# Performance work log

Measured on AMD Instinct MI355X. Metric: run time of the kernel, lower is better.

Reference implementation:

```python
import jax, jax.numpy as jnp
import numpy as np

H, D, E, S_E, P_E, N, B = 16, 48, 768, 384, 128, 768, 1

def _ln(x, g=None, b=None, eps=1e-5):
    mu = jnp.mean(x, axis=-1, keepdims=True)
    var = jnp.var(x, axis=-1, keepdims=True)
    y = (x - mu) * jax.lax.rsqrt(var + eps)
    if g is not None:
        y = y * g
    if b is not None:
        y = y + b
    return y

def setup_inputs() -> dict:
    key = jax.random.key(0)
    ks = jax.random.split(key, 16)
    sc_e = 1.0 / np.sqrt(E)
    sc_s = 1.0 / np.sqrt(S_E)
    sc_p = 1.0 / np.sqrt(P_E)
    return {
        "a": jax.random.normal(ks[0], (B, N, E), jnp.float32),
        "s": jax.random.normal(ks[1], (B, N, S_E), jnp.float32),
        "pair_rep": jax.random.normal(ks[2], (B, N, N, P_E), jnp.float32),
        "beta": jax.random.normal(ks[3], (B, N, N), jnp.float32),
        # AdaLN: sigmoid-gated scale and shift from s
        "w_ada_gamma": jax.random.normal(ks[4], (S_E, E), jnp.float32) * sc_s,
        "w_ada_beta": jax.random.normal(ks[5], (S_E, E), jnp.float32) * sc_s,
        # q/k/v projections, stored as [E, H, D]
        "wq": jax.random.normal(ks[6], (E, H, D), jnp.float32) * sc_e,
        "bq": jnp.zeros((H, D), jnp.float32),
        "wk": jax.random.normal(ks[7], (E, H, D), jnp.float32) * sc_e,
        "wv": jax.random.normal(ks[8], (E, H, D), jnp.float32) * sc_e,
        # pair bias: LayerNorm(P_E) + Linear(P_E -> H, no bias)
        "ln_pair_g": jnp.ones((P_E,), jnp.float32),
        "ln_pair_b": jnp.zeros((P_E,), jnp.float32),
        "w_pair": jax.random.normal(ks[9], (P_E, H), jnp.float32) * sc_p,
        # gate projection [E, H, D], no bias, sigmoid
        "w_gate": jax.random.normal(ks[10], (E, H, D), jnp.float32) * sc_e,
        # output projections
        "w_proj_a": jax.random.normal(ks[11], (E, E), jnp.float32) * sc_e,
        "w_out": jax.random.normal(ks[12], (S_E, E), jnp.float32) * sc_s,
        "b_out": jnp.full((E,), -2.0, jnp.float32),
    }

def reference(a, s, pair_rep, beta, w_ada_gamma, w_ada_beta, wq, bq, wk, wv,
              ln_pair_g, ln_pair_b, w_pair, w_gate, w_proj_a, w_out, b_out):
    # AdaLN: normalize a (no affine); gamma/beta conditioned on normalized s
    a_n = _ln(a)
    s_n = _ln(s)
    gamma = jax.nn.sigmoid(s_n @ w_ada_gamma)
    a_mod = gamma * a_n + s_n @ w_ada_beta            # [B,N,E]

    q = jnp.einsum('bne,ehd->bnhd', a_mod, wq) + bq   # [B,N,H,D]
    k = jnp.einsum('bne,ehd->bnhd', a_mod, wk)
    v = jnp.einsum('bne,ehd->bnhd', a_mod, wv)
    g = jax.nn.sigmoid(jnp.einsum('bne,ehd->bnhd', a_mod, w_gate))

    # per-head pair bias: LN(pair) @ w_pair + beta -> [B,H,N,N]
    b = jnp.einsum('bnmp,ph->bhnm', _ln(pair_rep, ln_pair_g, ln_pair_b), w_pair)
    b = b + beta[:, None, :, :]

    scale = 1.0 / np.sqrt(D)
    logits = jnp.einsum('bnhd,bmhd->bhnm', q, k) * scale + b
    weights = jax.nn.softmax(logits, axis=-1)         # [B,H,N,N]

    attn = jnp.einsum('bhnm,bmhd->bhnd', weights, v)
    attn = attn * jnp.moveaxis(g, -2, -3)             # gate per head
    attn = jnp.moveaxis(attn, -3, -2).reshape(a.shape[0], a.shape[1], H * D)
    out = attn @ w_proj_a                             # [B,N,E]
    out = jax.nn.sigmoid(s @ w_out + b_out) * out
    return out
```

## Files before the change

### kernel.cpp

```cpp
#include <hip/hip_runtime.h>
#include <hip/hip_bf16.h>

typedef __attribute__((ext_vector_type(8))) short short8;
typedef __attribute__((ext_vector_type(8))) unsigned short u16x8;
typedef __attribute__((ext_vector_type(4))) unsigned short u16x4;
typedef __attribute__((ext_vector_type(4))) float f32x4;
typedef __attribute__((ext_vector_type(4))) unsigned u32x4;

#define NTOK 768
#define ED   768
#define SD   384
#define PD   128
#define NH   16
#define DH   48
#define LGS  778

__device__ __forceinline__ unsigned short f2bf(float x) {
  unsigned u = __builtin_bit_cast(unsigned, x);
  u += 0x7FFFu + ((u >> 16) & 1u);
  return (unsigned short)(u >> 16);
}
__device__ __forceinline__ float bf2f(unsigned short b) {
  unsigned u = ((unsigned)b) << 16;
  return __builtin_bit_cast(float, u);
}
__device__ __forceinline__ float sigm(float x) { return 1.0f / (1.0f + __expf(-x)); }

__device__ __forceinline__ unsigned cvtpk(float a, float b) {
  unsigned r;
  asm("v_cvt_pk_bf16_f32 %0, %1, %2" : "=v"(r) : "v"(a), "v"(b));
  return r;
}
__device__ __forceinline__ float lo2f(unsigned p) {
  return __builtin_bit_cast(float, p << 16);
}
__device__ __forceinline__ float hi2f(unsigned p) {
  return __builtin_bit_cast(float, p & 0xFFFF0000u);
}

__device__ __forceinline__ void gl2lds(const unsigned short* g, unsigned short* l) {
  __builtin_amdgcn_global_load_lds(
      (const __attribute__((address_space(1))) unsigned int*)g,
      (__attribute__((address_space(3))) unsigned int*)l, 16, 0, 0);
}

constexpr size_t SZ_SN   = (size_t)NTOK * SD * 2;
constexpr size_t OFF_SNH = 0;
constexpr size_t OFF_SNL = OFF_SNH + SZ_SN;
constexpr size_t OFF_SRH = OFF_SNL + SZ_SN;
constexpr size_t OFF_SRL = OFF_SRH + SZ_SN;
constexpr size_t OFF_GAM = OFF_SRL + SZ_SN;
constexpr size_t OFF_BET = OFF_GAM + 2359296;
constexpr size_t OFF_OG  = OFF_BET + 2359296;
constexpr size_t OFF_AMH = OFF_OG  + 2359296;
constexpr size_t OFF_AML = OFF_AMH + 1179648;
constexpr size_t OFF_QB  = OFF_AML + 1179648;
constexpr size_t OFF_KB  = OFF_QB  + 1179648;
constexpr size_t OFF_VT  = OFF_KB  + 1179648;
constexpr size_t OFF_GBUF= OFF_VT  + 1179648;
constexpr size_t OFF_AGH = OFF_GBUF+ 2359296;
constexpr size_t OFF_AGL = OFF_AGH + 1179648;
constexpr size_t OFF_WSMH= OFF_AGL + 1179648;
constexpr size_t OFF_WSML= OFF_WSMH+ 1769472;
constexpr size_t OFF_WQH = OFF_WSML+ 1769472;
constexpr size_t OFF_WQL = OFF_WQH + 4718592;
constexpr size_t OFF_WPH = OFF_WQL + 4718592;
constexpr size_t OFF_WPL = OFF_WPH + 1179648;
constexpr size_t OFF_GWH = OFF_WPL + 1179648;
constexpr size_t OFF_GWL = OFF_GWH + 4096;
constexpr size_t OFF_SGW = OFF_GWL + 4096;
constexpr size_t OFF_QKL = OFF_SGW + 4096;
constexpr size_t OFF_PB  = OFF_QKL + 37748736;
constexpr size_t WS_NEED = OFF_PB  + 18874368;

__global__ __launch_bounds__(256) void k_wcvt(
    const float* __restrict__ wag, const float* __restrict__ wab, const float* __restrict__ wo,
    const float* __restrict__ wq, const float* __restrict__ wk, const float* __restrict__ wv,
    const float* __restrict__ wg, const float* __restrict__ wp,
    const float* __restrict__ lng, const float* __restrict__ lnb,
    const float* __restrict__ wpair, const float* __restrict__ s,
    unsigned short* __restrict__ wsmh, unsigned short* __restrict__ wsml,
    unsigned short* __restrict__ wqh, unsigned short* __restrict__ wql,
    unsigned short* __restrict__ wph, unsigned short* __restrict__ wpl,
    unsigned short* __restrict__ gwh, unsigned short* __restrict__ gwl,
    float* __restrict__ sgw, float* __restrict__ bw,
    unsigned short* __restrict__ snh, unsigned short* __restrict__ snl,
    unsigned short* __restrict__ srh, unsigned short* __restrict__ srl) {
  const int tid = threadIdx.x;
  if (blockIdx.z == 8) {
    const int gid = blockIdx.y * 24 + blockIdx.x;
    if (gid == 192) {
      if (tid < 128) {
        float g = lng[tid];
        for (int hh = 0; hh < 16; ++hh) {
          float gwv = g * wpair[tid * 16 + hh];
          unsigned short hb = f2bf(gwv);
          gwh[tid * 16 + hh] = hb;
          gwl[tid * 16 + hh] = f2bf(gwv - bf2f(hb));
        }
      }
      if (tid < 16) {
        float sv = 0.f, bb = 0.f;
        for (int p = 0; p < 128; ++p) {
          float w = wpair[p * 16 + tid];
          sv += lng[p] * w;
          bb += lnb[p] * w;
        }
        sgw[tid] = sv;
        bw[tid]  = bb;
      }
      return;
    }
    if (gid > 192) return;
    const int n = gid * 4 + (tid >> 6);
    const int lane = tid & 63;
    const float* row = s + (size_t)n * SD;
    float v[6], sum = 0.f, sq = 0.f;
#pragma unroll
    for (int i = 0; i < 6; ++i) { v[i] = row[lane + 64 * i]; sum += v[i]; sq += v[i] * v[i]; }
#pragma unroll
    for (int off = 1; off < 64; off <<= 1) { sum += __shfl_xor(sum, off); sq += __shfl_xor(sq, off); }
    float mu = sum * (1.f / SD);
    float var = sq * (1.f / SD) - mu * mu;
    float rs = rsqrtf(var + 1e-5f);
#pragma unroll
    for (int i = 0; i < 6; ++i) {
      size_t idx = (size_t)n * SD + lane + 64 * i;
      float x = v[i];
      unsigned short xh = f2bf(x);
      srh[idx] = xh; srl[idx] = f2bf(x - bf2f(xh));
      float y = (x - mu) * rs;
      unsigned short yh = f2bf(y);
      snh[idx] = yh; snl[idx] = f2bf(y - bf2f(yh));
    }
    return;
  }
  const int id = blockIdx.z;
  const float* src; int Ksrc; unsigned short *dh, *dl; int n0; int Kd;
  switch (id) {
    case 0: src = wag; Ksrc = 384; dh = wsmh; dl = wsml; n0 = 0;    Kd = 384; break;
    case 1: src = wab; Ksrc = 384; dh = wsmh; dl = wsml; n0 = 768;  Kd = 384; break;
    case 2: src = wo;  Ksrc = 384; dh = wsmh; dl = wsml; n0 = 1536; Kd = 384; break;
    case 3: src = wq;  Ksrc = 768; dh = wqh;  dl = wql;  n0 = 0;    Kd = 768; break;
    case 4: src = wk;  Ksrc = 768; dh = wqh;  dl = wql;  n0 = 768;  Kd = 768; break;
    case 5: src = wv;  Ksrc = 768; dh = wqh;  dl = wql;  n0 = 1536; Kd = 768; break;
    case 6: src = wg;  Ksrc = 768; dh = wqh;  dl = wql;  n0 = 2304; Kd = 768; break;
    default: src = wp; Ksrc = 768; dh = wph;  dl = wpl;  n0 = 0;    Kd = 768; break;
  }
  const int kt = blockIdx.x, ntile = blockIdx.y;
  if (kt * 32 >= Ksrc) return;
  __shared__ float t[32][33];
  const int r = tid >> 3, c4 = (tid & 7) * 4;
  float4 v = *(const float4*)(src + (size_t)(kt * 32 + r) * 768 + ntile * 32 + c4);
  t[r][c4 + 0] = v.x; t[r][c4 + 1] = v.y; t[r][c4 + 2] = v.z; t[r][c4 + 3] = v.w;
  __syncthreads();
  u16x4 hv, lv;
#pragma unroll
  for (int j = 0; j < 4; ++j) {
    float x = t[c4 + j][r];
    unsigned short hb = f2bf(x);
    hv[j] = hb;
    lv[j] = f2bf(x - bf2f(hb));
  }
  size_t drow = (size_t)(n0 + ntile * 32 + r) * Kd + kt * 32 + c4;
  *(u16x4*)(dh + drow) = hv;
  *(u16x4*)(dl + drow) = lv;
}

__device__ __forceinline__ void mfma_core(
    const unsigned short* __restrict__ Ah, const unsigned short* __restrict__ Al,
    const unsigned short* __restrict__ Bh, const unsigned short* __restrict__ Bl,
    int K, int mBase, int nBase, f32x4 acc[2][2]) {
  __shared__ unsigned short lds[2][4][4096];
  const int tid = threadIdx.x;
  const int w = tid >> 6, lane = tid & 63;
  const int l15 = lane & 15, kg = lane >> 4;
  const int wr = w >> 1, wc = w & 1;

  size_t offA[2], offB[2];
  int ldsw[2];
#pragma unroll
  for (int i = 0; i < 2; ++i) {
    int chunk = w * 128 + i * 64 + lane;
    int row = chunk >> 3;
    int slot = (chunk & 7) ^ (row & 7);
    offA[i] = (size_t)(mBase + row) * K + slot * 8;
    offB[i] = (size_t)(nBase + row) * K + slot * 8;
    ldsw[i] = w * 1024 + i * 512;
  }
  auto stage = [&](int b, int k0) {
#pragma unroll
    for (int i = 0; i < 2; ++i) {
      gl2lds(Ah + offA[i] + k0, &lds[b][0][ldsw[i]]);
      gl2lds(Al + offA[i] + k0, &lds[b][1][ldsw[i]]);
      gl2lds(Bh + offB[i] + k0, &lds[b][2][ldsw[i]]);
      gl2lds(Bl + offB[i] + k0, &lds[b][3][ldsw[i]]);
    }
  };

  stage(0, 0);
  int buf = 0;
  for (int k0 = 64; k0 <= K; k0 += 64) {
    __syncthreads();
    if (k0 < K) stage(buf ^ 1, k0);
#pragma unroll
    for (int kk = 0; kk < 2; ++kk) {
      short8 ah[2], al[2], bh4[2], bl4[2];
#pragma unroll
      for (int mi = 0; mi < 2; ++mi) {
        int row = wr * 32 + mi * 16 + l15;
        int kb = kk * 64 + kg * 16;
        int idx = row * 64 + ((kb ^ ((row & 7) << 4)) >> 1);
        ah[mi] = *(const short8*)&lds[buf][0][idx];
        al[mi] = *(const short8*)&lds[buf][1][idx];
      }
#pragma unroll
      for (int ni = 0; ni < 2; ++ni) {
        int row = wc * 32 + ni * 16 + l15;
        int kb = kk * 64 + kg * 16;
        int idx = row * 64 + ((kb ^ ((row & 7) << 4)) >> 1);
        bh4[ni] = *(const short8*)&lds[buf][2][idx];
        bl4[ni] = *(const short8*)&lds[buf][3][idx];
      }
#pragma unroll
      for (int mi = 0; mi < 2; ++mi)
#pragma unroll
        for (int ni = 0; ni < 2; ++ni) {
          acc[mi][ni] = __builtin_amdgcn_mfma_f32_16x16x32_bf16(ah[mi], bh4[ni], acc[mi][ni], 0, 0, 0);
          acc[mi][ni] = __builtin_amdgcn_mfma_f32_16x16x32_bf16(al[mi], bh4[ni], acc[mi][ni], 0, 0, 0);
          acc[mi][ni] = __builtin_amdgcn_mfma_f32_16x16x32_bf16(ah[mi], bl4[ni], acc[mi][ni], 0, 0, 0);
        }
    }
    buf ^= 1;
  }
}

__global__ __launch_bounds__(256) void k_gemm_small(
    const unsigned short* __restrict__ snh, const unsigned short* __restrict__ snl,
    const unsigned short* __restrict__ srh, const unsigned short* __restrict__ srl,
    const unsigned short* __restrict__ wsmh, const unsigned short* __restrict__ wsml,
    const float* __restrict__ bo,
    float* __restrict__ gaml, float* __restrict__ betl, float* __restrict__ og) {
  const int nt = blockIdx.x, mt = blockIdx.y;
  const unsigned short* Ah = (nt < 24) ? snh : srh;
  const unsigned short* Al = (nt < 24) ? snl : srl;
  f32x4 acc[2][2];
#pragma unroll
  for (int i = 0; i < 2; ++i)
#pragma unroll
    for (int j = 0; j < 2; ++j) acc[i][j] = (f32x4){0.f, 0.f, 0.f, 0.f};
  mfma_core(Ah, Al, wsmh, wsml, SD, mt * 64, nt * 64, acc);
  const int tid = threadIdx.x;
  const int w = tid >> 6, lane = tid & 63;
  const int l15 = lane & 15, kg = lane >> 4;
  const int wr = w >> 1, wc = w & 1;
#pragma unroll
  for (int mi = 0; mi < 2; ++mi)
#pragma unroll
    for (int ni = 0; ni < 2; ++ni) {
      int col = nt * 64 + wc * 32 + ni * 16 + l15;
#pragma unroll
      for (int r = 0; r < 4; ++r) {
        int row = mt * 64 + wr * 32 + mi * 16 + kg * 4 + r;
        float v = acc[mi][ni][r];
        if (col < 768) gaml[(size_t)row * ED + col] = v;
        else if (col < 1536) betl[(size_t)row * ED + col - 768] = v;
        else og[(size_t)row * ED + col - 1536] = sigm(v + bo[col - 1536]);
      }
    }
}

__global__ __launch_bounds__(256) void k_gemm_qkvg(
    const unsigned short* __restrict__ amh, const unsigned short* __restrict__ aml,
    const unsigned short* __restrict__ wqh, const unsigned short* __restrict__ wql,
    const float* __restrict__ bq,
    unsigned short* __restrict__ qb, unsigned short* __restrict__ kb,
    unsigned short* __restrict__ vT, float* __restrict__ gbuf) {
  const int nt = blockIdx.x, mt = blockIdx.y;
  f32x4 acc[2][2];
#pragma unroll
  for (int i = 0; i < 2; ++i)
#pragma unroll
    for (int j = 0; j < 2; ++j) acc[i][j] = (f32x4){0.f, 0.f, 0.f, 0.f};
  mfma_core(amh, aml, wqh, wql, ED, mt * 64, nt * 64, acc);
  const int tid = threadIdx.x;
  const int w = tid >> 6, lane = tid & 63;
  const int l15 = lane & 15, kg = lane >> 4;
  const int wr = w >> 1, wc = w & 1;
  const int sel = nt / 12;
#pragma unroll
  for (int mi = 0; mi < 2; ++mi)
#pragma unroll
    for (int ni = 0; ni < 2; ++ni) {
      int col = nt * 64 + wc * 32 + ni * 16 + l15;
      int c = col - sel * 768;
#pragma unroll
      for (int r = 0; r < 4; ++r) {
        int row = mt * 64 + wr * 32 + mi * 16 + kg * 4 + r;
        float v = acc[mi][ni][r];
        size_t idx = (size_t)row * ED + c;
        if (sel == 0) qb[idx] = f2bf(v + bq[c]);
        else if (sel == 1) kb[idx] = f2bf(v);
        else if (sel == 2) vT[(size_t)c * NTOK + row] = f2bf(v);
        else gbuf[idx] = sigm(v);
      }
    }
}

__global__ __launch_bounds__(256) void k_gemm_proj(
    const unsigned short* __restrict__ agh, const unsigned short* __restrict__ agl,
    const unsigned short* __restrict__ wph, const unsigned short* __restrict__ wpl,
    const float* __restrict__ og, float* __restrict__ out) {
  const int nt = blockIdx.x, mt = blockIdx.y;
  f32x4 acc[2][2];
#pragma unroll
  for (int i = 0; i < 2; ++i)
#pragma unroll
    for (int j = 0; j < 2; ++j) acc[i][j] = (f32x4){0.f, 0.f, 0.f, 0.f};
  mfma_core(agh, agl, wph, wpl, ED, mt * 64, nt * 64, acc);
  const int tid = threadIdx.x;
  const int w = tid >> 6, lane = tid & 63;
  const int l15 = lane & 15, kg = lane >> 4;
  const int wr = w >> 1, wc = w & 1;
#pragma unroll
  for (int mi = 0; mi < 2; ++mi)
#pragma unroll
    for (int ni = 0; ni < 2; ++ni) {
      int col = nt * 64 + wc * 32 + ni * 16 + l15;
#pragma unroll
      for (int r = 0; r < 4; ++r) {
        int row = mt * 64 + wr * 32 + mi * 16 + kg * 4 + r;
        size_t idx = (size_t)row * ED + col;
        out[idx] = acc[mi][ni][r] * og[idx];
      }
    }
}

__global__ __launch_bounds__(256) void k_amod(const float* __restrict__ a,
                                              const float* __restrict__ gamma_lin,
                                              const float* __restrict__ beta_lin,
                                              unsigned short* __restrict__ amh,
                                              unsigned short* __restrict__ aml) {
  __shared__ float red[8];
  const int n = blockIdx.x, tid = threadIdx.x;
  const int lane = tid & 63, wid = tid >> 6;
  const float* row = a + (size_t)n * ED;
  float v[3], sum = 0.f, sq = 0.f;
#pragma unroll
  for (int i = 0; i < 3; ++i) { v[i] = row[tid + 256 * i]; sum += v[i]; sq += v[i] * v[i]; }
#pragma unroll
  for (int off = 1; off < 64; off <<= 1) { sum += __shfl_xor(sum, off); sq += __shfl_xor(sq, off); }
  if (lane == 0) { red[wid] = sum; red[4 + wid] = sq; }
  __syncthreads();
  float S = red[0] + red[1] + red[2] + red[3];
  float Q = red[4] + red[5] + red[6] + red[7];
  float mu = S * (1.f / ED);
  float var = Q * (1.f / ED) - mu * mu;
  float rs = rsqrtf(var + 1e-5f);
#pragma unroll
  for (int i = 0; i < 3; ++i) {
    int e = tid + 256 * i;
    float an = (v[i] - mu) * rs;
    size_t idx = (size_t)n * ED + e;
    float val = sigm(gamma_lin[idx]) * an + beta_lin[idx];
    unsigned short h = f2bf(val);
    amh[idx] = h;
    aml[idx] = f2bf(val - bf2f(h));
  }
}

__global__ __launch_bounds__(256) void k_qkw(const unsigned short* __restrict__ qb,
                                             const unsigned short* __restrict__ kb,
                                             const float* __restrict__ beta,
                                             float* __restrict__ qkl) {
  const int mt = blockIdx.x, ntile = blockIdx.y, h = blockIdx.z;
  __shared__ unsigned short qs[64 * 72];
  __shared__ unsigned short ksm[64 * 72];
  const int tid = threadIdx.x;
  const int n0 = ntile * 64, m0 = mt * 64;
  const u16x8 z = {0, 0, 0, 0, 0, 0, 0, 0};
#pragma unroll
  for (int it = 0; it < 2; ++it) {
    int idx = tid + it * 256;
    int row = idx >> 3, c = idx & 7;
    u16x8 vq = z, vk = z;
    if (c < 6) {
      vq = *(const u16x8*)(qb + (size_t)(n0 + row) * ED + h * DH + c * 8);
      vk = *(const u16x8*)(kb + (size_t)(m0 + row) * ED + h * DH + c * 8);
    }
    *(u16x8*)(qs + row * 72 + c * 8) = vq;
    *(u16x8*)(ksm + row * 72 + c * 8) = vk;
  }
  __syncthreads();
  const int wv = tid >> 6, lane = tid & 63;
  const int l15 = lane & 15, kg = lane >> 4;
  f32x4 acc[4];
#pragma unroll
  for (int ct = 0; ct < 4; ++ct) acc[ct] = (f32x4){0.f, 0.f, 0.f, 0.f};
#pragma unroll
  for (int ks2 = 0; ks2 < 2; ++ks2) {
    short8 av = *(const short8*)(qs + (wv * 16 + l15) * 72 + ks2 * 32 + kg * 8);
#pragma unroll
    for (int ct = 0; ct < 4; ++ct) {
      short8 bv = *(const short8*)(ksm + (ct * 16 + l15) * 72 + ks2 * 32 + kg * 8);
      acc[ct] = __builtin_amdgcn_mfma_f32_16x16x32_bf16(av, bv, acc[ct], 0, 0, 0);
    }
  }
  const float scale = 0.14433756729740643f;
#pragma unroll
  for (int ct = 0; ct < 4; ++ct)
#pragma unroll
    for (int r = 0; r < 4; ++r) {
      int nn = n0 + wv * 16 + kg * 4 + r;
      int mm = m0 + ct * 16 + l15;
      qkl[((size_t)nn * NH + h) * NTOK + mm] =
          fmaf(acc[ct][r], scale, beta[(size_t)nn * NTOK + mm]);
    }
}

__global__ __launch_bounds__(256, 3) void k_pairsm(const float* __restrict__ pair_rep,
                                                   const float* __restrict__ qkl,
                                                   const unsigned short* __restrict__ gw_hi,
                                                   const unsigned short* __restrict__ gw_lo,
                                                   const float* __restrict__ sgw, const float* __restrict__ bw,
                                                   unsigned short* __restrict__ pb) {
  __shared__ float lg[16 * LGS];
  const int n = blockIdx.x;
  const int tid = threadIdx.x;
  const int wv = tid >> 6, lane = tid & 63;
  const int l15 = lane & 15, kg = lane >> 4;

#define LOADCH(X, CH) do {                                                        \
    const float* xp_ = pair_rep + ((size_t)n * NTOK + (CH) * 16 + l15) * PD + kg * 8; \
    _Pragma("unroll")                                                             \
    for (int q_ = 0; q_ < 4; ++q_) {                                              \
      X[q_ * 2]     = *(const float4*)(xp_ + q_ * 32);                            \
      X[q_ * 2 + 1] = *(const float4*)(xp_ + q_ * 32 + 4);                        \
    }                                                                             \
  } while (0)

  float4 Xa[8], Xb[8];
  LOADCH(Xa, wv);
  LOADCH(Xb, wv + 4);

  short8 bh[4], bl[4];
#pragma unroll
  for (int ks = 0; ks < 4; ++ks)
#pragma unroll
    for (int j = 0; j < 8; ++j) {
      int p = ks * 32 + kg * 8 + j;
      bh[ks][j] = (short)gw_hi[p * 16 + l15];
      bl[ks][j] = (short)gw_lo[p * 16 + l15];
    }
  float sgv[4], bwv[4];
#pragma unroll
  for (int r = 0; r < 4; ++r) { sgv[r] = sgw[kg * 4 + r]; bwv[r] = bw[kg * 4 + r]; }

#define PROC(X, CH) do {                                                          \
    float sum_ = 0.f, sq_ = 0.f;                                                  \
    _Pragma("unroll")                                                             \
    for (int q_ = 0; q_ < 8; ++q_) {                                              \
      sum_ += X[q_].x + X[q_].y + X[q_].z + X[q_].w;                              \
      sq_ = fmaf(X[q_].x, X[q_].x, sq_); sq_ = fmaf(X[q_].y, X[q_].y, sq_);       \
      sq_ = fmaf(X[q_].z, X[q_].z, sq_); sq_ = fmaf(X[q_].w, X[q_].w, sq_);       \
    }                                                                             \
    sum_ += __shfl_xor(sum_, 16); sum_ += __shfl_xor(sum_, 32);                   \
    sq_  += __shfl_xor(sq_, 16);  sq_  += __shfl_xor(sq_, 32);                    \
    float mu_ = sum_ * (1.f / 128.f);                                             \
    float rstd_ = rsqrtf(sq_ * (1.f / 128.f) - mu_ * mu_ + 1e-5f);                \
    f32x4 acc_ = {0.f, 0.f, 0.f, 0.f};                                            \
    _Pragma("unroll")                                                             \
    for (int ks_ = 0; ks_ < 4; ++ks_) {                                           \
      float4 u0_ = X[ks_ * 2], u1_ = X[ks_ * 2 + 1];                              \
      unsigned p0_ = cvtpk(u0_.x, u0_.y), p1_ = cvtpk(u0_.z, u0_.w);              \
      unsigned p2_ = cvtpk(u1_.x, u1_.y), p3_ = cvtpk(u1_.z, u1_.w);              \
      float l0_ = u0_.x - lo2f(p0_), l1_ = u0_.y - hi2f(p0_);                     \
      float l2_ = u0_.z - lo2f(p1_), l3_ = u0_.w - hi2f(p1_);                     \
      float l4_ = u1_.x - lo2f(p2_), l5_ = u1_.y - hi2f(p2_);                     \
      float l6_ = u1_.z - lo2f(p3_), l7_ = u1_.w - hi2f(p3_);                     \
      unsigned q0_ = cvtpk(l0_, l1_), q1_ = cvtpk(l2_, l3_);                      \
      unsigned q2_ = cvtpk(l4_, l5_), q3_ = cvtpk(l6_, l7_);                      \
      u32x4 hp_ = {p0_, p1_, p2_, p3_}, lp_ = {q0_, q1_, q2_, q3_};               \
      short8 ah_ = __builtin_bit_cast(short8, hp_);                               \
      short8 al_ = __builtin_bit_cast(short8, lp_);                               \
      acc_ = __builtin_amdgcn_mfma_f32_16x16x32_bf16(bh[ks_], ah_, acc_, 0, 0, 0);\
      acc_ = __builtin_amdgcn_mfma_f32_16x16x32_bf16(bh[ks_], al_, acc_, 0, 0, 0);\
      acc_ = __builtin_amdgcn_mfma_f32_16x16x32_bf16(bl[ks_], ah_, acc_, 0, 0, 0);\
    }                                                                             \
    _Pragma("unroll")                                                             \
    for (int r_ = 0; r_ < 4; ++r_) {                                              \
      float val_ = rstd_ * (acc_[r_] - mu_ * sgv[r_]) + bwv[r_];                  \
      lg[(kg * 4 + r_) * LGS + (CH) * 16 + l15] = val_;                           \
    }                                                                             \
  } while (0)

  PROC(Xa, wv +  0); LOADCH(Xa, wv +  8);
  PROC(Xb, wv +  4); LOADCH(Xb, wv + 12);
  PROC(Xa, wv +  8); LOADCH(Xa, wv + 16);
  PROC(Xb, wv + 12); LOADCH(Xb, wv + 20);
  PROC(Xa, wv + 16); LOADCH(Xa, wv + 24);
  PROC(Xb, wv + 20); LOADCH(Xb, wv + 28);
  PROC(Xa, wv + 24); LOADCH(Xa, wv + 32);
  PROC(Xb, wv + 28); LOADCH(Xb, wv + 36);
  PROC(Xa, wv + 32); LOADCH(Xa, wv + 40);
  PROC(Xb, wv + 36); LOADCH(Xb, wv + 44);
  PROC(Xa, wv + 40);
  PROC(Xb, wv + 44);
#undef LOADCH
#undef PROC
  __syncthreads();

#pragma unroll
  for (int hh = 0; hh < 4; ++hh) {
    int h = wv * 4 + hh;
    const float* qrow = qkl + ((size_t)n * NH + h) * NTOK;
    float x[12];
#pragma unroll
    for (int i = 0; i < 12; ++i) x[i] = lg[h * LGS + lane + 64 * i] + qrow[lane + 64 * i];
    float mx = x[0];
#pragma unroll
    for (int t = 1; t < 12; ++t) mx = fmaxf(mx, x[t]);
#pragma unroll
    for (int off = 1; off < 64; off <<= 1) mx = fmaxf(mx, __shfl_xor(mx, off));
    float e[12], sm = 0.f;
#pragma unroll
    for (int t = 0; t < 12; ++t) { e[t] = __expf(x[t] - mx); sm += e[t]; }
#pragma unroll
    for (int off = 1; off < 64; off <<= 1) sm += __shfl_xor(sm, off);
    float inv = 1.0f / sm;
    unsigned short* dst = pb + ((size_t)h * NTOK + n) * NTOK;
#pragma unroll
    for (int i = 0; i < 12; ++i) dst[lane + 64 * i] = f2bf(e[i] * inv);
  }
}

__global__ __launch_bounds__(256) void k_pv(const unsigned short* __restrict__ wb,
                                            const unsigned short* __restrict__ vT,
                                            const float* __restrict__ gbuf,
                                            unsigned short* __restrict__ agh,
                                            unsigned short* __restrict__ agl) {
  const int ntile = blockIdx.x, h = blockIdx.y;
  const int n0 = ntile * 64;
  __shared__ unsigned short wsm[64 * 40];
  __shared__ unsigned short vtm[48 * 40];
  const int tid = threadIdx.x;
  const int wv = tid >> 6, lane = tid & 63, l15 = lane & 15, kg = lane >> 4;
  f32x4 acc[3];
#pragma unroll
  for (int dt = 0; dt < 3; ++dt) acc[dt] = (f32x4){0.f, 0.f, 0.f, 0.f};
  for (int k0 = 0; k0 < NTOK; k0 += 32) {
    __syncthreads();
    {
      int row = tid >> 2, c = tid & 3;
      *(u16x8*)(wsm + row * 40 + c * 8) =
          *(const u16x8*)(wb + ((size_t)h * NTOK + (n0 + row)) * NTOK + k0 + c * 8);
    }
    if (tid < 192) {
      int d = tid >> 2, c = tid & 3;
      *(u16x8*)(vtm + d * 40 + c * 8) =
          *(const u16x8*)(vT + (size_t)(h * DH + d) * NTOK + k0 + c * 8);
    }
    __syncthreads();
    short8 av = *(const short8*)(wsm + (wv * 16 + l15) * 40 + kg * 8);
#pragma unroll
    for (int dt = 0; dt < 3; ++dt) {
      short8 bv = *(const short8*)(vtm + (dt * 16 + l15) * 40 + kg * 8);
      acc[dt] = __builtin_amdgcn_mfma_f32_16x16x32_bf16(av, bv, acc[dt], 0, 0, 0);
    }
  }
#pragma unroll
  for (int dt = 0; dt < 3; ++dt)
#pragma unroll
    for (int r = 0; r < 4; ++r) {
      int nn = n0 + wv * 16 + kg * 4 + r;
      int col = h * DH + dt * 16 + l15;
      size_t idx = (size_t)nn * ED + col;
      float val = acc[dt][r] * gbuf[idx];
      unsigned short hb = f2bf(val);
      agh[idx] = hb;
      agl[idx] = f2bf(val - bf2f(hb));
    }
}

extern "C" void kernel_launch(void* const* d_in, const int* in_sizes, int n_in,
                              void* d_out, int out_size, void* d_ws, size_t ws_size,
                              hipStream_t stream) {
  const float* a    = (const float*)d_in[0];
  const float* s    = (const float*)d_in[1];
  const float* pair = (const float*)d_in[2];
  const float* beta = (const float*)d_in[3];
  const float* wag  = (const float*)d_in[4];
  const float* wab  = (const float*)d_in[5];
  const float* wq   = (const float*)d_in[6];
  const float* bq   = (const float*)d_in[7];
  const float* wk   = (const float*)d_in[8];
  const float* wvp  = (const float*)d_in[9];
  const float* lng  = (const float*)d_in[10];
  const float* lnb  = (const float*)d_in[11];
  const float* wpair= (const float*)d_in[12];
  const float* wg   = (const float*)d_in[13];
  const float* wproj= (const float*)d_in[14];
  const float* wo   = (const float*)d_in[15];
  const float* bo   = (const float*)d_in[16];
  float* out = (float*)d_out;

  if (ws_size < WS_NEED) return;

  char* ws = (char*)d_ws;
  unsigned short* snh  = (unsigned short*)(ws + OFF_SNH);
  unsigned short* snl  = (unsigned short*)(ws + OFF_SNL);
  unsigned short* srh  = (unsigned short*)(ws + OFF_SRH);
  unsigned short* srl  = (unsigned short*)(ws + OFF_SRL);
  float*          gaml = (float*)(ws + OFF_GAM);
  float*          betl = (float*)(ws + OFF_BET);
  float*          og   = (float*)(ws + OFF_OG);
  unsigned short* amh  = (unsigned short*)(ws + OFF_AMH);
  unsigned short* aml  = (unsigned short*)(ws + OFF_AML);
  unsigned short* qb   = (unsigned short*)(ws + OFF_QB);
  unsigned short* kb   = (unsigned short*)(ws + OFF_KB);
  unsigned short* vT   = (unsigned short*)(ws + OFF_VT);
  float*          gbuf = (float*)(ws + OFF_GBUF);
  unsigned short* agh  = (unsigned short*)(ws + OFF_AGH);
  unsigned short* agl  = (unsigned short*)(ws + OFF_AGL);
  unsigned short* wsmh = (unsigned short*)(ws + OFF_WSMH);
  unsigned short* wsml = (unsigned short*)(ws + OFF_WSML);
  unsigned short* wqh  = (unsigned short*)(ws + OFF_WQH);
  unsigned short* wql  = (unsigned short*)(ws + OFF_WQL);
  unsigned short* wph  = (unsigned short*)(ws + OFF_WPH);
  unsigned short* wpl  = (unsigned short*)(ws + OFF_WPL);
  unsigned short* gwh  = (unsigned short*)(ws + OFF_GWH);
  unsigned short* gwl  = (unsigned short*)(ws + OFF_GWL);
  float*          sgw  = (float*)(ws + OFF_SGW);
  float*          bw   = sgw + 16;
  float*          qkl  = (float*)(ws + OFF_QKL);
  unsigned short* pb   = (unsigned short*)(ws + OFF_PB);

  hipLaunchKernelGGL(k_wcvt, dim3(24, 24, 9), dim3(256), 0, stream,
                     wag, wab, wo, wq, wk, wvp, wg, wproj, lng, lnb, wpair, s,
                     wsmh, wsml, wqh, wql, wph, wpl, gwh, gwl, sgw, bw,
                     snh, snl, srh, srl);
  hipLaunchKernelGGL(k_gemm_small, dim3(36, 12), dim3(256), 0, stream,
                     snh, snl, srh, srl, wsmh, wsml, bo, gaml, betl, og);
  hipLaunchKernelGGL(k_amod, dim3(768), dim3(256), 0, stream, a, gaml, betl, amh, aml);
  hipLaunchKernelGGL(k_gemm_qkvg, dim3(48, 12), dim3(256), 0, stream,
                     amh, aml, wqh, wql, bq, qb, kb, vT, gbuf);
  hipLaunchKernelGGL(k_qkw, dim3(12, 12, 16), dim3(256), 0, stream, qb, kb, beta, qkl);
  hipLaunchKernelGGL(k_pairsm, dim3(768), dim3(256), 0, stream,
                     pair, qkl, gwh, gwl, sgw, bw, pb);
  hipLaunchKernelGGL(k_pv, dim3(12, 16), dim3(256), 0, stream, pb, vT, gbuf, agh, agl);
  hipLaunchKernelGGL(k_gemm_proj, dim3(12, 12), dim3(256), 0, stream,
                     agh, agl, wph, wpl, og, out);
}
```

Measured before the change: 172.2 us.

## Enlarge QK tile to 128x128 and make PV single-wave without LDS staging

The QK logits kernel moves from 64x64 to 128x128 tiles, with each wave computing a 64x64 sub-tile from register-held A fragments. This raises MFMA reuse per LDS load and cuts the block count. The PV kernel now uses one 64-thread wave per 16 rows per head and reads probabilities and V fragments straight from global memory. That removes the LDS staging and barriers and gives more blocks (768 instead of 192) to fill the GPU, at the cost of uncoalesced-ish direct global reads and more register pressure in QK.

New measurement: 176.3 us. +2.4%, slower.

```diff
diff --git a/kernel.cpp b/kernel.cpp
--- a/kernel.cpp
+++ b/kernel.cpp
@@ -374,13 +374,13 @@
                                              const float* __restrict__ beta,
                                              float* __restrict__ qkl) {
   const int mt = blockIdx.x, ntile = blockIdx.y, h = blockIdx.z;
-  __shared__ unsigned short qs[64 * 72];
-  __shared__ unsigned short ksm[64 * 72];
+  __shared__ unsigned short qs[128 * 72];
+  __shared__ unsigned short ksm[128 * 72];
   const int tid = threadIdx.x;
-  const int n0 = ntile * 64, m0 = mt * 64;
+  const int n0 = ntile * 128, m0 = mt * 128;
   const u16x8 z = {0, 0, 0, 0, 0, 0, 0, 0};
 #pragma unroll
-  for (int it = 0; it < 2; ++it) {
+  for (int it = 0; it < 4; ++it) {
     int idx = tid + it * 256;
     int row = idx >> 3, c = idx & 7;
     u16x8 vq = z, vk = z;
@@ -392,30 +392,40 @@
     *(u16x8*)(ksm + row * 72 + c * 8) = vk;
   }
   __syncthreads();
-  const int wv = tid >> 6, lane = tid & 63;
+  const int w = tid >> 6, lane = tid & 63;
   const int l15 = lane & 15, kg = lane >> 4;
-  f32x4 acc[4];
-#pragma unroll
-  for (int ct = 0; ct < 4; ++ct) acc[ct] = (f32x4){0.f, 0.f, 0.f, 0.f};
+  const int wn = w >> 1, wm = w & 1;
+  f32x4 acc[4][4];
+#pragma unroll
+  for (int i = 0; i < 4; ++i)
+#pragma unroll
+    for (int j = 0; j < 4; ++j) acc[i][j] = (f32x4){0.f, 0.f, 0.f, 0.f};
 #pragma unroll
   for (int ks2 = 0; ks2 < 2; ++ks2) {
-    short8 av = *(const short8*)(qs + (wv * 16 + l15) * 72 + ks2 * 32 + kg * 8);
-#pragma unroll
-    for (int ct = 0; ct < 4; ++ct) {
-      short8 bv = *(const short8*)(ksm + (ct * 16 + l15) * 72 + ks2 * 32 + kg * 8);
-      acc[ct] = __builtin_amdgcn_mfma_f32_16x16x32_bf16(av, bv, acc[ct], 0, 0, 0);
+    short8 av[4];
+#pragma unroll
+    for (int ni = 0; ni < 4; ++ni)
+      av[ni] = *(const short8*)(qs + (wn * 64 + ni * 16 + l15) * 72 + ks2 * 32 + kg * 8);
+#pragma unroll
+    for (int mj = 0; mj < 4; ++mj) {
+      short8 bv = *(const short8*)(ksm + (wm * 64 + mj * 16 + l15) * 72 + ks2 * 32 + kg * 8);
+#pragma unroll
+      for (int ni = 0; ni < 4; ++ni)
+        acc[ni][mj] = __builtin_amdgcn_mfma_f32_16x16x32_bf16(av[ni], bv, acc[ni][mj], 0, 0, 0);
     }
   }
   const float scale = 0.14433756729740643f;
 #pragma unroll
-  for (int ct = 0; ct < 4; ++ct)
-#pragma unroll
-    for (int r = 0; r < 4; ++r) {
-      int nn = n0 + wv * 16 + kg * 4 + r;
-      int mm = m0 + ct * 16 + l15;
-      qkl[((size_t)nn * NH + h) * NTOK + mm] =
-          fmaf(acc[ct][r], scale, beta[(size_t)nn * NTOK + mm]);
-    }
+  for (int ni = 0; ni < 4; ++ni)
+#pragma unroll
+    for (int mj = 0; mj < 4; ++mj)
+#pragma unroll
+      for (int r = 0; r < 4; ++r) {
+        int nn = n0 + wn * 64 + ni * 16 + kg * 4 + r;
+        int mm = m0 + wm * 64 + mj * 16 + l15;
+        qkl[((size_t)nn * NH + h) * NTOK + mm] =
+            fmaf(acc[ni][mj][r], scale, beta[(size_t)nn * NTOK + mm]);
+      }
 }
 
 __global__ __launch_bounds__(256, 3) void k_pairsm(const float* __restrict__ pair_rep,
@@ -534,45 +544,37 @@
   }
 }
 
-__global__ __launch_bounds__(256) void k_pv(const unsigned short* __restrict__ wb,
-                                            const unsigned short* __restrict__ vT,
-                                            const float* __restrict__ gbuf,
-                                            unsigned short* __restrict__ agh,
-                                            unsigned short* __restrict__ agl) {
-  const int ntile = blockIdx.x, h = blockIdx.y;
-  const int n0 = ntile * 64;
-  __shared__ unsigned short wsm[64 * 40];
-  __shared__ unsigned short vtm[48 * 40];
-  const int tid = threadIdx.x;
-  const int wv = tid >> 6, lane = tid & 63, l15 = lane & 15, kg = lane >> 4;
+__global__ __launch_bounds__(64) void k_pv(const unsigned short* __restrict__ wb,
+                                           const unsigned short* __restrict__ vT,
+                                           const float* __restrict__ gbuf,
+                                           unsigned short* __restrict__ agh,
+                                           unsigned short* __restrict__ agl) {
+  const int nt16 = blockIdx.x, h = blockIdx.y;
+  const int n0 = nt16 * 16;
+  const int lane = threadIdx.x;
+  const int l15 = lane & 15, kg = lane >> 4;
   f32x4 acc[3];
 #pragma unroll
   for (int dt = 0; dt < 3; ++dt) acc[dt] = (f32x4){0.f, 0.f, 0.f, 0.f};
-  for (int k0 = 0; k0 < NTOK; k0 += 32) {
-    __syncthreads();
-    {
-      int row = tid >> 2, c = tid & 3;
-      *(u16x8*)(wsm + row * 40 + c * 8) =
-          *(const u16x8*)(wb + ((size_t)h * NTOK + (n0 + row)) * NTOK + k0 + c * 8);
-    }
-    if (tid < 192) {
-      int d = tid >> 2, c = tid & 3;
-      *(u16x8*)(vtm + d * 40 + c * 8) =
-          *(const u16x8*)(vT + (size_t)(h * DH + d) * NTOK + k0 + c * 8);
-    }
-    __syncthreads();
-    short8 av = *(const short8*)(wsm + (wv * 16 + l15) * 40 + kg * 8);
-#pragma unroll
-    for (int dt = 0; dt < 3; ++dt) {
-      short8 bv = *(const short8*)(vtm + (dt * 16 + l15) * 40 + kg * 8);
-      acc[dt] = __builtin_amdgcn_mfma_f32_16x16x32_bf16(av, bv, acc[dt], 0, 0, 0);
+  const unsigned short* prow = wb + ((size_t)h * NTOK + n0 + l15) * NTOK + kg * 8;
+  const unsigned short* vrow0 = vT + (size_t)(h * DH + l15) * NTOK + kg * 8;
+  for (int k0 = 0; k0 < NTOK; k0 += 64) {
+#pragma unroll
+    for (int ks2 = 0; ks2 < 2; ++ks2) {
+      int kofs = k0 + ks2 * 32;
+      short8 av = *(const short8*)(prow + kofs);
+#pragma unroll
+      for (int dt = 0; dt < 3; ++dt) {
+        short8 bv = *(const short8*)(vrow0 + (size_t)dt * 16 * NTOK + kofs);
+        acc[dt] = __builtin_amdgcn_mfma_f32_16x16x32_bf16(av, bv, acc[dt], 0, 0, 0);
+      }
     }
   }
 #pragma unroll
   for (int dt = 0; dt < 3; ++dt)
 #pragma unroll
     for (int r = 0; r < 4; ++r) {
-      int nn = n0 + wv * 16 + kg * 4 + r;
+      int nn = n0 + kg * 4 + r;
       int col = h * DH + dt * 16 + l15;
       size_t idx = (size_t)nn * ED + col;
       float val = acc[dt][r] * gbuf[idx];
@@ -644,10 +646,10 @@
   hipLaunchKernelGGL(k_amod, dim3(768), dim3(256), 0, stream, a, gaml, betl, amh, aml);
   hipLaunchKernelGGL(k_gemm_qkvg, dim3(48, 12), dim3(256), 0, stream,
                      amh, aml, wqh, wql, bq, qb, kb, vT, gbuf);
-  hipLaunchKernelGGL(k_qkw, dim3(12, 12, 16), dim3(256), 0, stream, qb, kb, beta, qkl);
+  hipLaunchKernelGGL(k_qkw, dim3(6, 6, 16), dim3(256), 0, stream, qb, kb, beta, qkl);
   hipLaunchKernelGGL(k_pairsm, dim3(768), dim3(256), 0, stream,
                      pair, qkl, gwh, gwl, sgw, bw, pb);
-  hipLaunchKernelGGL(k_pv, dim3(12, 16), dim3(256), 0, stream, pb, vT, gbuf, agh, agl);
+  hipLaunchKernelGGL(k_pv, dim3(48, 16), dim3(64), 0, stream, pb, vT, gbuf, agh, agl);
   hipLaunchKernelGGL(k_gemm_proj, dim3(12, 12), dim3(256), 0, stream,
                      agh, agl, wph, wpl, og, out);
 }
```
